# Kernel tuning notes

Measured on AMD Instinct MI355X. Metric: run time of the kernel, lower is better.

## Reference

```python
import jax, jax.numpy as jnp
import numpy as np
from jax import lax

GRID_SIZE = 5
SPLINE_ORDER = 3
N_COEF = GRID_SIZE + SPLINE_ORDER  # 8 b-spline basis functions per input
GRID_LO, GRID_HI = -1.0, 1.0


def _grid():
    h = (GRID_HI - GRID_LO) / GRID_SIZE
    return jnp.arange(-SPLINE_ORDER, GRID_SIZE + SPLINE_ORDER + 1, dtype=jnp.float32) * h + GRID_LO


def _bsplines(x):
    # x: [..., in] -> [..., in, N_COEF] via Cox-de Boor recursion (efficient-kan)
    grid = _grid()
    x = x[..., None]
    bases = ((x >= grid[:-1]) & (x < grid[1:])).astype(x.dtype)
    for j in range(1, SPLINE_ORDER + 1):
        bases = ((x - grid[:-(j + 1)]) / (grid[j:-1] - grid[:-(j + 1)]) * bases[..., :-1]
                 + (grid[j + 1:] - x) / (grid[j + 1:] - grid[1:-j]) * bases[..., 1:])
    return bases


def _kan_linear(x, base_w, spline_w):
    # x: [..., in]; base_w: [out, in]; spline_w: [out, in, N_COEF]
    base = jax.nn.silu(x) @ base_w.T
    b = _bsplines(x).reshape(x.shape[:-1] + (-1,))  # [..., in*N_COEF]
    return base + b @ spline_w.reshape(spline_w.shape[0], -1).T


def _kan_conv(x, base_w, spline_w):
    # x: [B, C, H, W]; 3x3 valid KAN convolution
    patches = lax.conv_general_dilated_patches(x, (3, 3), (1, 1), 'VALID')  # [B, C*9, H-2, W-2]
    p = patches.transpose(0, 2, 3, 1)  # [B, Ho, Wo, C*9]
    out = _kan_linear(p, base_w, spline_w)  # [B, Ho, Wo, out]
    return out.transpose(0, 3, 1, 2)


def _maxpool2(x):
    return lax.reduce_window(x, -jnp.inf, lax.max, (1, 1, 2, 2), (1, 1, 2, 2), 'VALID')


def setup_inputs() -> dict:
    key = jax.random.key(0)
    ks = jax.random.split(key, 12)
    B = 2048
    x = jax.random.uniform(ks[0], (B, 1, 28, 28), dtype=jnp.float32)
    s = 0.1
    return {
        'x': x,
        'bw1': jax.random.normal(ks[1], (5, 9), dtype=jnp.float32) * s,
        'sw1': jax.random.normal(ks[2], (5, 9, N_COEF), dtype=jnp.float32) * s,
        'bw2': jax.random.normal(ks[3], (5, 45), dtype=jnp.float32) * s,
        'sw2': jax.random.normal(ks[4], (5, 45, N_COEF), dtype=jnp.float32) * s,
        'bw3': jax.random.normal(ks[5], (2, 45), dtype=jnp.float32) * s,
        'sw3': jax.random.normal(ks[6], (2, 45, N_COEF), dtype=jnp.float32) * s,
        'w1': jax.random.normal(ks[7], (500, 162), dtype=jnp.float32) * 0.05,
        'b1': jnp.zeros((500,), dtype=jnp.float32),
        'w2': jax.random.normal(ks[8], (10, 500), dtype=jnp.float32) * 0.05,
        'b2': jnp.zeros((10,), dtype=jnp.float32),
    }


def reference(x, bw1, sw1, bw2, sw2, bw3, sw3, w1, b1, w2, b2):
    h = _kan_conv(x, bw1, sw1)       # [B, 5, 26, 26]
    h = _maxpool2(h)                 # [B, 5, 13, 13]
    h = _kan_conv(h, bw2, sw2)       # [B, 5, 11, 11]
    h = _kan_conv(h, bw3, sw3)       # [B, 2, 9, 9]
    h = h.reshape(h.shape[0], -1)    # [B, 162]
    h = jax.nn.relu(h @ w1.T + b1)   # [B, 500]
    return h @ w2.T + b2             # [B, 10]
```

## Files before the change

### kernel.cpp

```cpp
#include <hip/hip_runtime.h>


typedef _Float16 h2 __attribute__((ext_vector_type(2)));
typedef _Float16 f16x8 __attribute__((ext_vector_type(8)));
typedef float f32x4 __attribute__((ext_vector_type(4)));

union U4H { uint4 u; f16x8 h; };

__device__ __forceinline__ h2 u2h(unsigned int u) {
  union { unsigned int x; h2 h; } v; v.x = u; return v.h;
}
__device__ __forceinline__ unsigned short f2h_bits(float x) {
  union { _Float16 h; unsigned short u; } v; v.h = (_Float16)x; return v.u;
}
__device__ __forceinline__ float h2f(unsigned short u) {
  union { unsigned short u; _Float16 h; } v; v.u = u; return (float)v.h;
}
__device__ __forceinline__ unsigned int pack2h(float a, float b) {
  return (unsigned int)f2h_bits(a) | ((unsigned int)f2h_bits(b) << 16);
}
__device__ __forceinline__ float fdot2(h2 a, h2 b, float c) {
  return __builtin_amdgcn_fdot2(a, b, c, false);
}

__device__ __forceinline__ constexpr int off1(int t) {
  return (t / 3) * 28 + (t % 3);
}
__device__ __forceinline__ constexpr int off2v(int t) {
  return (t / 9) * 169 + ((t % 9) / 3) * 13 + ((t % 9) % 3);
}

__device__ __forceinline__ void featurize_regs(float v, uint4& bs, float& silu) {
  silu = v / (1.0f + __expf(-v));
  bs.x = 0u; bs.y = 0u; bs.z = 0u; bs.w = 0u;
  float u = fmaf(v, 2.5f, 5.5f);
  if (u >= 0.0f && u < 11.0f) {
    float tf = floorf(u);
    float f = u - tf, f2 = f * f, f3 = f2 * f, om = 1.0f - f;
    const float c6 = 1.0f / 6.0f;
    float w0 = om * om * om * c6;
    float w1 = (3.0f * f3 - 6.0f * f2 + 4.0f) * c6;
    float w2 = (-3.0f * f3 + 3.0f * f2 + 3.0f * f + 1.0f) * c6;
    float w3 = f3 * c6;
    unsigned long long w01 =
        (unsigned long long)f2h_bits(w0) |
        ((unsigned long long)f2h_bits(w1) << 16) |
        ((unsigned long long)f2h_bits(w2) << 32) |
        ((unsigned long long)f2h_bits(w3) << 48);
    int t = (int)tf;
    int s = 16 * t - 48;
    unsigned long long lo, hi;
    if (s >= 0) {
      lo = (s < 64) ? (w01 << s) : 0ull;
      hi = (s == 0) ? 0ull : ((s < 64) ? (w01 >> (64 - s)) : (w01 << (s - 64)));
    } else {
      lo = w01 >> (-s);
      hi = 0ull;
    }
    bs.x = (unsigned int)lo; bs.y = (unsigned int)(lo >> 32);
    bs.z = (unsigned int)hi; bs.w = (unsigned int)(hi >> 32);
  }
}

template <int NO, int CHS, int ROWW>
__device__ __forceinline__ void kconv_plain(
    const uint4* bas, const unsigned short* slu,
    const uint4* __restrict__ wS, const float* __restrict__ wB,
    int y0, int x0, float (&acc)[NO]) {
  const uint4* wp = wS;
  const float* bp = wB;
  int baC = y0 * ROWW + x0;
  #pragma unroll 1
  for (int c = 0; c < 5; ++c) {
    int ba = baC;
    #pragma unroll 1
    for (int ky = 0; ky < 3; ++ky) {
      uint4 q0 = bas[ba], q1 = bas[ba + 1], q2 = bas[ba + 2];
      float s0 = h2f(slu[ba]), s1 = h2f(slu[ba + 1]), s2 = h2f(slu[ba + 2]);
      #pragma unroll
      for (int kx = 0; kx < 3; ++kx) {
        uint4 q = (kx == 0) ? q0 : ((kx == 1) ? q1 : q2);
        float sl = (kx == 0) ? s0 : ((kx == 1) ? s1 : s2);
        h2 a0 = u2h(q.x), a1 = u2h(q.y), a2 = u2h(q.z), a3 = u2h(q.w);
        #pragma unroll
        for (int j = 0; j < NO; ++j) {
          uint4 w = wp[kx * NO + j];
          float a = acc[j];
          a = fdot2(a0, u2h(w.x), a);
          a = fdot2(a1, u2h(w.y), a);
          a = fdot2(a2, u2h(w.z), a);
          a = fdot2(a3, u2h(w.w), a);
          acc[j] = fmaf(sl, bp[kx * NO + j], a);
        }
      }
      wp += 3 * NO; bp += 3 * NO;
      ba += ROWW;
    }
    baC += CHS;
  }
}

__global__ __launch_bounds__(256) void k_prep(
    const float* __restrict__ bw1, const float* __restrict__ sw1,
    const float* __restrict__ bw2, const float* __restrict__ sw2,
    const float* __restrict__ bw3, const float* __restrict__ sw3,
    const float* __restrict__ w1, const float* __restrict__ w2,
    unsigned int* __restrict__ Bc1g, unsigned int* __restrict__ B2g,
    unsigned int* __restrict__ V3Gs, float* __restrict__ V3Gb,
    unsigned int* __restrict__ W1p4, float* __restrict__ W2p) {
  int t = blockIdx.x * 256 + threadIdx.x;
  if (t < 1280) {
    int i = t & 3, l = (t >> 2) & 63, s = t >> 8;
    int k = s * 32 + ((l >> 4) & 3) * 8 + 2 * i;
    int col = l & 15, tap = k >> 4, slot = k & 15;
    unsigned int v = 0u;
    if (col < 5 && tap < 9) {
      if (slot < 8) {
        const float* sp = sw1 + (col * 9 + tap) * 8 + slot;
        v = pack2h(sp[0], sp[1]);
      } else if (slot == 8) {
        float bv = bw1[col * 9 + tap];
        float hi = (float)(_Float16)bv;
        v = pack2h(hi, bv - hi);
      }
    }
    Bc1g[t] = v;
  }
  if (t < 5888) {
    int i = t & 3, l = (t >> 2) & 63, s = t >> 8;
    int k = s * 32 + ((l >> 4) & 3) * 8 + 2 * i;
    int col = l & 15, tap = k >> 4, slot = k & 15;
    unsigned int v = 0u;
    if (col < 5 && tap < 45) {
      if (slot < 8) {
        const float* sp = sw2 + (col * 45 + tap) * 8 + slot;
        v = pack2h(sp[0], sp[1]);
      } else if (slot == 8) {
        float bv = bw2[col * 45 + tap];
        float hi = (float)(_Float16)bv;
        v = pack2h(hi, bv - hi);
      }
    }
    B2g[t] = v;
  }
  if (t < 360) {
    int p = t & 3, u4 = t >> 2;
    int kx = u4 % 3, cky = (u4 / 3) % 15, ou = u4 / 45;
    int in = (cky / 3) * 9 + (cky % 3) * 3 + kx;
    V3Gs[t] = pack2h(sw3[(ou * 45 + in) * 8 + 2 * p], sw3[(ou * 45 + in) * 8 + 2 * p + 1]);
  }
  if (t < 90) {
    int kx = t % 3, cky = (t / 3) % 15, ou = t / 45;
    int in = (cky / 3) * 9 + (cky % 3) * 3 + kx;
    V3Gb[t] = bw3[ou * 45 + in];
  }
  if (t < 43008) {
    int j = t & 3, o = (t >> 2) & 511, g = t >> 11;
    int kp = g * 4 + j;
    W1p4[t] = (o < 500 && kp < 81)
                  ? pack2h(w1[o * 162 + 2 * kp], w1[o * 162 + 2 * kp + 1])
                  : 0u;
  }
  if (t < 5120) {
    int o = t >> 9, k = t & 511;
    W2p[t] = (k < 500) ? w2[o * 500 + k] : 0.0f;
  }
}

__global__ __launch_bounds__(256, 6) void k_fused(
    const float* __restrict__ x,
    const unsigned int* __restrict__ Bc1g, const unsigned int* __restrict__ B2g,
    const unsigned int* __restrict__ V3Gs, const float* __restrict__ V3Gb,
    const unsigned int* __restrict__ W1p4, const float* __restrict__ W2p,
    const float* __restrict__ b1, const float* __restrict__ b2,
    float* __restrict__ out) {
  __shared__ __attribute__((aligned(16))) char pool[23680];
  uint4*          RECB = (uint4*)pool;
  unsigned int*   INSP = (unsigned int*)(pool + 12544);
  uint4*          H1B  = (uint4*)pool;
  unsigned int*   H1SP = (unsigned int*)(pool + 13520);
  unsigned short* WRES = (unsigned short*)(pool + 16900);
  float*          C2   = (float*)(pool + 16900);
  uint4*          H2B  = (uint4*)pool;
  unsigned short* SLU2 = (unsigned short*)(pool + 9680);
  float*          H3F  = (float*)(pool + 16900);
  unsigned int*   HPK  = (unsigned int*)(pool + 17552);
  float*          RED  = (float*)(pool + 17888);
  unsigned int*   ZERO = (unsigned int*)(pool + 23664);
  float*          BASF = (float*)pool;

  const int b   = blockIdx.x;
  const int tid = threadIdx.x;
  const int lane = tid & 63;
  const int wv   = tid >> 6;
  const int col  = lane & 15;
  const int hi4  = lane >> 4;
  const int haf  = hi4 & 1;
  const int par  = hi4 >> 1;

  if (tid < 4) ZERO[tid] = 0u;
  #pragma unroll 1
  for (int l = tid; l < 784; l += 256) {
    uint4 bs; float sl;
    featurize_regs(x[b * 784 + l], bs, sl);
    RECB[l] = bs; INSP[l] = pack2h(sl, sl);
  }
  __syncthreads();

  {
    U4H B1[5];
    #pragma unroll
    for (int s = 0; s < 5; ++s)
      B1[s].u = ((const uint4*)Bc1g)[s * 64 + lane];
    int mt0 = wv * 11;
    int mtn = (wv < 3) ? 11 : 10;
    #pragma unroll 1
    for (int m = 0; m < mtn; ++m) {
      int mt = mt0 + m;
      int w = mt * 16 + col;
      int wc = (w < 676) ? w : 675;
      int wy = wc / 26;
      int wbase = wy * 28 + (wc - wy * 26);
      f32x4 acc = {0.f, 0.f, 0.f, 0.f};
      #pragma unroll
      for (int s = 0; s < 5; ++s) {
        const int toV = 2 * s + 1;
        int roff = par ? ((toV < 9) ? off1(toV) : 0) : off1(2 * s);
        bool valid = (!par) || (toV < 9);
        U4H a;
        if (haf == 0) {
          const uint4* ap = valid ? (RECB + (wbase + roff)) : (const uint4*)ZERO;
          a.u = *ap;
        } else {
          const unsigned int* sp = valid ? (INSP + (wbase + roff)) : ZERO;
          a.u.x = *sp; a.u.y = 0u; a.u.z = 0u; a.u.w = 0u;
        }
        acc = __builtin_amdgcn_mfma_f32_16x16x32_f16(a.h, B1[s].h, acc, 0, 0, 0);
      }
      if (col < 5) {
        #pragma unroll
        for (int r = 0; r < 4; ++r) {
          int wr = mt * 16 + hi4 * 4 + r;
          if (wr < 676) WRES[col * 676 + wr] = f2h_bits(acc[r]);
        }
      }
    }
  }
  __syncthreads();

  if (tid < 169) {
    int py = tid / 13, px = tid - (tid / 13) * 13;
    int w00 = py * 52 + px * 2;
    const unsigned int* W32 = (const unsigned int*)WRES;
    #pragma unroll
    for (int o = 0; o < 5; ++o) {
      unsigned int a = W32[(o * 676 + w00) >> 1];
      unsigned int c = W32[(o * 676 + w00 + 26) >> 1];
      float v = fmaxf(fmaxf(h2f((unsigned short)a), h2f((unsigned short)(a >> 16))),
                      fmaxf(h2f((unsigned short)c), h2f((unsigned short)(c >> 16))));
      uint4 bs; float sl;
      featurize_regs(v, bs, sl);
      H1B[o * 169 + tid] = bs;
      H1SP[o * 169 + tid] = pack2h(sl, sl);
    }
  }
  __syncthreads();

  {
    int p0 = (wv * 2) * 16 + col;
    int p1 = (wv * 2 + 1) * 16 + col;
    int pc0 = (p0 < 121) ? p0 : 120;
    int pc1 = (p1 < 121) ? p1 : 120;
    int y0 = pc0 / 11, pb0 = y0 * 13 + (pc0 - y0 * 11);
    int y1 = pc1 / 11, pb1 = y1 * 13 + (pc1 - y1 * 11);
    f32x4 ac0 = {0.f, 0.f, 0.f, 0.f}, ac1 = {0.f, 0.f, 0.f, 0.f};
    #pragma unroll
    for (int s = 0; s < 23; ++s) {
      const int toV = 2 * s + 1;
      int roff = par ? ((toV < 45) ? off2v(toV) : 0) : off2v(2 * s);
      bool valid = (!par) || (toV < 45);
      U4H bf; bf.u = ((const uint4*)B2g)[s * 64 + lane];
      U4H a0, a1;
      if (haf == 0) {
        const uint4* q0 = valid ? (H1B + (pb0 + roff)) : (const uint4*)ZERO;
        const uint4* q1 = valid ? (H1B + (pb1 + roff)) : (const uint4*)ZERO;
        a0.u = *q0; a1.u = *q1;
      } else {
        const unsigned int* s0p = valid ? (H1SP + (pb0 + roff)) : ZERO;
        const unsigned int* s1p = valid ? (H1SP + (pb1 + roff)) : ZERO;
        a0.u.x = *s0p; a0.u.y = 0u; a0.u.z = 0u; a0.u.w = 0u;
        a1.u.x = *s1p; a1.u.y = 0u; a1.u.z = 0u; a1.u.w = 0u;
      }
      ac0 = __builtin_amdgcn_mfma_f32_16x16x32_f16(a0.h, bf.h, ac0, 0, 0, 0);
      ac1 = __builtin_amdgcn_mfma_f32_16x16x32_f16(a1.h, bf.h, ac1, 0, 0, 0);
    }
    if (col < 5) {
      #pragma unroll
      for (int r = 0; r < 4; ++r) {
        C2[col * 128 + (wv * 2) * 16 + hi4 * 4 + r]     = ac0[r];
        C2[col * 128 + (wv * 2 + 1) * 16 + hi4 * 4 + r] = ac1[r];
      }
    }
  }
  __syncthreads();

  #pragma unroll 1
  for (int k2 = 0; k2 < 3; ++k2) {
    int it = tid + 256 * k2;
    if (it < 605) {
      int o = it / 121, p = it - o * 121;
      uint4 bs; float sl;
      featurize_regs(C2[o * 128 + p], bs, sl);
      H2B[o * 121 + p] = bs;
      SLU2[o * 121 + p] = f2h_bits(sl);
    }
  }
  __syncthreads();

  int og = __builtin_amdgcn_readfirstlane(tid >> 7);
  int p2 = tid & 127;
  float acc3[1] = {0.0f};
  {
    int pc = (p2 < 81) ? p2 : 80;
    int y0 = pc / 9, x0 = pc - (pc / 9) * 9;
    kconv_plain<1, 121, 11>(H2B, SLU2, (const uint4*)V3Gs + og * 45,
                            V3Gb + og * 45, y0, x0, acc3);
  }
  if (p2 < 81) H3F[og * 81 + p2] = acc3[0];
  __syncthreads();
  if (tid < 84)
    HPK[tid] = (tid < 81) ? pack2h(H3F[2 * tid], H3F[2 * tid + 1]) : 0u;
  __syncthreads();

  float fa[2] = {0.0f, 0.0f};
  {
    const uint4* hp4 = (const uint4*)HPK;
    const uint4* wbase = (const uint4*)W1p4 + tid;
    uint4 wA[2], wB[2];
    #pragma unroll
    for (int i = 0; i < 2; ++i) wA[i] = wbase[i * 256];
    #pragma unroll 1
    for (int g = 0; g < 21; g += 2) {
      if (g + 1 < 21) {
        const uint4* p = wbase + (g + 1) * 512;
        #pragma unroll
        for (int i = 0; i < 2; ++i) wB[i] = p[i * 256];
      }
      {
        uint4 hk = hp4[g];
        #pragma unroll
        for (int i = 0; i < 2; ++i) {
          float a = fa[i];
          a = fdot2(u2h(hk.x), u2h(wA[i].x), a);
          a = fdot2(u2h(hk.y), u2h(wA[i].y), a);
          a = fdot2(u2h(hk.z), u2h(wA[i].z), a);
          a = fdot2(u2h(hk.w), u2h(wA[i].w), a);
          fa[i] = a;
        }
      }
      if (g + 2 < 21) {
        const uint4* p = wbase + (g + 2) * 512;
        #pragma unroll
        for (int i = 0; i < 2; ++i) wA[i] = p[i * 256];
      }
      if (g + 1 < 21) {
        uint4 hk = hp4[g + 1];
        #pragma unroll
        for (int i = 0; i < 2; ++i) {
          float a = fa[i];
          a = fdot2(u2h(hk.x), u2h(wB[i].x), a);
          a = fdot2(u2h(hk.y), u2h(wB[i].y), a);
          a = fdot2(u2h(hk.z), u2h(wB[i].z), a);
          a = fdot2(u2h(hk.w), u2h(wB[i].w), a);
          fa[i] = a;
        }
      }
    }
  }
  #pragma unroll
  for (int i = 0; i < 2; ++i) {
    int o = tid + 256 * i;
    float bb = (o < 500) ? b1[o] : 0.0f;
    float v = fa[i] + bb;
    BASF[o] = (v > 0.0f && o < 500) ? v : 0.0f;
  }
  __syncthreads();

  float acc10[10];
  {
    float2 ha = ((const float2*)BASF)[tid];
    #pragma unroll
    for (int o = 0; o < 10; ++o) {
      float2 w = ((const float2*)&W2p[o * 512])[tid];
      acc10[o] = ha.x * w.x + ha.y * w.y;
    }
  }
  #pragma unroll
  for (int off = 32; off > 0; off >>= 1) {
    #pragma unroll
    for (int o = 0; o < 10; ++o) acc10[o] += __shfl_down(acc10[o], off);
  }
  if ((tid & 63) == 0) {
    int wid = tid >> 6;
    #pragma unroll
    for (int o = 0; o < 10; ++o) RED[wid * 10 + o] = acc10[o];
  }
  __syncthreads();
  if (tid < 10)
    out[b * 10 + tid] = RED[tid] + RED[10 + tid] + RED[20 + tid] + RED[30 + tid] + b2[tid];
}

extern "C" void kernel_launch(void* const* d_in, const int* in_sizes, int n_in,
                              void* d_out, int out_size, void* d_ws, size_t ws_size,
                              hipStream_t stream) {
  (void)in_sizes; (void)n_in; (void)out_size; (void)ws_size;
  const float* x   = (const float*)d_in[0];
  const float* bw1 = (const float*)d_in[1];
  const float* sw1 = (const float*)d_in[2];
  const float* bw2 = (const float*)d_in[3];
  const float* sw2 = (const float*)d_in[4];
  const float* bw3 = (const float*)d_in[5];
  const float* sw3 = (const float*)d_in[6];
  const float* w1  = (const float*)d_in[7];
  const float* b1  = (const float*)d_in[8];
  const float* w2  = (const float*)d_in[9];
  const float* b2  = (const float*)d_in[10];
  float* out = (float*)d_out;

  char* ws = (char*)d_ws;
  unsigned int* Bc1g = (unsigned int*)(ws);
  unsigned int* B2g  = (unsigned int*)(ws + 5120);
  unsigned int* V3Gs = (unsigned int*)(ws + 28672);
  float*        V3Gb = (float*)(ws + 30112);
  float*        W2p  = (float*)(ws + 30720);
  unsigned int* W1p4 = (unsigned int*)(ws + 51200);

  k_prep<<<168, 256, 0, stream>>>(bw1, sw1, bw2, sw2, bw3, sw3, w1, w2,
                                  Bc1g, B2g, V3Gs, V3Gb, W1p4, W2p);
  k_fused<<<2048, 256, 0, stream>>>(x, Bc1g, B2g, V3Gs, V3Gb,
                                    W1p4, W2p, b1, b2, out);
}
```

Before: 130.5 us.

## Move third KAN conv to MFMA and drop zero-pointer select in tap loops

Replaces the scalar fdot2-based third KAN convolution with a 16x16x32 f16 MFMA implicit-GEMM over 81 positions, using a packed B3 weight matrix prepared in k_prep that holds spline and split-precision base weights. Stores silu values duplicated as packed half pairs so the hi/lo base weight trick works in the MFMA k-slot. Also simplifies the tap offset computation for conv1/conv2 by mapping padded taps to offset 0 instead of selecting a zero buffer, relying on zero weights to null them. This moves layer-3 work onto the matrix cores but pads 2 outputs to 16 columns, wasting most of each MFMA, and leaves waves unevenly loaded across two passes.

Measured after the change: 137.4 us. +5.3%, slower.

```diff
diff --git a/kernel.cpp b/kernel.cpp
--- a/kernel.cpp
+++ b/kernel.cpp
@@ -23,11 +23,14 @@
   return __builtin_amdgcn_fdot2(a, b, c, false);
 }
 
-__device__ __forceinline__ constexpr int off1(int t) {
-  return (t / 3) * 28 + (t % 3);
-}
-__device__ __forceinline__ constexpr int off2v(int t) {
-  return (t / 9) * 169 + ((t % 9) / 3) * 13 + ((t % 9) % 3);
+__device__ __forceinline__ constexpr int off1t(int t) {
+  return (t >= 9) ? 0 : (t / 3) * 28 + (t % 3);
+}
+__device__ __forceinline__ constexpr int off2t(int t) {
+  return (t >= 45) ? 0 : (t / 9) * 169 + ((t % 9) / 3) * 13 + (t % 9) % 3;
+}
+__device__ __forceinline__ constexpr int off3t(int t) {
+  return (t >= 45) ? 0 : (t / 9) * 121 + ((t % 9) / 3) * 11 + (t % 9) % 3;
 }
 
 __device__ __forceinline__ void featurize_regs(float v, uint4& bs, float& silu) {
@@ -62,51 +65,13 @@
   }
 }
 
-template <int NO, int CHS, int ROWW>
-__device__ __forceinline__ void kconv_plain(
-    const uint4* bas, const unsigned short* slu,
-    const uint4* __restrict__ wS, const float* __restrict__ wB,
-    int y0, int x0, float (&acc)[NO]) {
-  const uint4* wp = wS;
-  const float* bp = wB;
-  int baC = y0 * ROWW + x0;
-  #pragma unroll 1
-  for (int c = 0; c < 5; ++c) {
-    int ba = baC;
-    #pragma unroll 1
-    for (int ky = 0; ky < 3; ++ky) {
-      uint4 q0 = bas[ba], q1 = bas[ba + 1], q2 = bas[ba + 2];
-      float s0 = h2f(slu[ba]), s1 = h2f(slu[ba + 1]), s2 = h2f(slu[ba + 2]);
-      #pragma unroll
-      for (int kx = 0; kx < 3; ++kx) {
-        uint4 q = (kx == 0) ? q0 : ((kx == 1) ? q1 : q2);
-        float sl = (kx == 0) ? s0 : ((kx == 1) ? s1 : s2);
-        h2 a0 = u2h(q.x), a1 = u2h(q.y), a2 = u2h(q.z), a3 = u2h(q.w);
-        #pragma unroll
-        for (int j = 0; j < NO; ++j) {
-          uint4 w = wp[kx * NO + j];
-          float a = acc[j];
-          a = fdot2(a0, u2h(w.x), a);
-          a = fdot2(a1, u2h(w.y), a);
-          a = fdot2(a2, u2h(w.z), a);
-          a = fdot2(a3, u2h(w.w), a);
-          acc[j] = fmaf(sl, bp[kx * NO + j], a);
-        }
-      }
-      wp += 3 * NO; bp += 3 * NO;
-      ba += ROWW;
-    }
-    baC += CHS;
-  }
-}
-
 __global__ __launch_bounds__(256) void k_prep(
     const float* __restrict__ bw1, const float* __restrict__ sw1,
     const float* __restrict__ bw2, const float* __restrict__ sw2,
     const float* __restrict__ bw3, const float* __restrict__ sw3,
     const float* __restrict__ w1, const float* __restrict__ w2,
     unsigned int* __restrict__ Bc1g, unsigned int* __restrict__ B2g,
-    unsigned int* __restrict__ V3Gs, float* __restrict__ V3Gb,
+    unsigned int* __restrict__ B3g,
     unsigned int* __restrict__ W1p4, float* __restrict__ W2p) {
   int t = blockIdx.x * 256 + threadIdx.x;
   if (t < 1280) {
@@ -143,16 +108,22 @@
     }
     B2g[t] = v;
   }
-  if (t < 360) {
-    int p = t & 3, u4 = t >> 2;
-    int kx = u4 % 3, cky = (u4 / 3) % 15, ou = u4 / 45;
-    int in = (cky / 3) * 9 + (cky % 3) * 3 + kx;
-    V3Gs[t] = pack2h(sw3[(ou * 45 + in) * 8 + 2 * p], sw3[(ou * 45 + in) * 8 + 2 * p + 1]);
-  }
-  if (t < 90) {
-    int kx = t % 3, cky = (t / 3) % 15, ou = t / 45;
-    int in = (cky / 3) * 9 + (cky % 3) * 3 + kx;
-    V3Gb[t] = bw3[ou * 45 + in];
+  if (t < 5888) {
+    int i = t & 3, l = (t >> 2) & 63, s = t >> 8;
+    int k = s * 32 + ((l >> 4) & 3) * 8 + 2 * i;
+    int col = l & 15, tap = k >> 4, slot = k & 15;
+    unsigned int v = 0u;
+    if (col < 2 && tap < 45) {
+      if (slot < 8) {
+        const float* sp = sw3 + (col * 45 + tap) * 8 + slot;
+        v = pack2h(sp[0], sp[1]);
+      } else if (slot == 8) {
+        float bv = bw3[col * 45 + tap];
+        float hi = (float)(_Float16)bv;
+        v = pack2h(hi, bv - hi);
+      }
+    }
+    B3g[t] = v;
   }
   if (t < 43008) {
     int j = t & 3, o = (t >> 2) & 511, g = t >> 11;
@@ -170,7 +141,7 @@
 __global__ __launch_bounds__(256, 6) void k_fused(
     const float* __restrict__ x,
     const unsigned int* __restrict__ Bc1g, const unsigned int* __restrict__ B2g,
-    const unsigned int* __restrict__ V3Gs, const float* __restrict__ V3Gb,
+    const unsigned int* __restrict__ B3g,
     const unsigned int* __restrict__ W1p4, const float* __restrict__ W2p,
     const float* __restrict__ b1, const float* __restrict__ b2,
     float* __restrict__ out) {
@@ -182,11 +153,10 @@
   unsigned short* WRES = (unsigned short*)(pool + 16900);
   float*          C2   = (float*)(pool + 16900);
   uint4*          H2B  = (uint4*)pool;
-  unsigned short* SLU2 = (unsigned short*)(pool + 9680);
+  unsigned int*   SP2  = (unsigned int*)(pool + 9680);
   float*          H3F  = (float*)(pool + 16900);
   unsigned int*   HPK  = (unsigned int*)(pool + 17552);
   float*          RED  = (float*)(pool + 17888);
-  unsigned int*   ZERO = (unsigned int*)(pool + 23664);
   float*          BASF = (float*)pool;
 
   const int b   = blockIdx.x;
@@ -198,7 +168,6 @@
   const int haf  = hi4 & 1;
   const int par  = hi4 >> 1;
 
-  if (tid < 4) ZERO[tid] = 0u;
   #pragma unroll 1
   for (int l = tid; l < 784; l += 256) {
     uint4 bs; float sl;
@@ -224,16 +193,12 @@
       f32x4 acc = {0.f, 0.f, 0.f, 0.f};
       #pragma unroll
       for (int s = 0; s < 5; ++s) {
-        const int toV = 2 * s + 1;
-        int roff = par ? ((toV < 9) ? off1(toV) : 0) : off1(2 * s);
-        bool valid = (!par) || (toV < 9);
+        int ro = par ? off1t(2 * s + 1) : off1t(2 * s);
         U4H a;
         if (haf == 0) {
-          const uint4* ap = valid ? (RECB + (wbase + roff)) : (const uint4*)ZERO;
-          a.u = *ap;
+          a.u = RECB[wbase + ro];
         } else {
-          const unsigned int* sp = valid ? (INSP + (wbase + roff)) : ZERO;
-          a.u.x = *sp; a.u.y = 0u; a.u.z = 0u; a.u.w = 0u;
+          a.u.x = INSP[wbase + ro]; a.u.y = 0u; a.u.z = 0u; a.u.w = 0u;
         }
         acc = __builtin_amdgcn_mfma_f32_16x16x32_f16(a.h, B1[s].h, acc, 0, 0, 0);
       }
@@ -276,20 +241,14 @@
     f32x4 ac0 = {0.f, 0.f, 0.f, 0.f}, ac1 = {0.f, 0.f, 0.f, 0.f};
     #pragma unroll
     for (int s = 0; s < 23; ++s) {
-      const int toV = 2 * s + 1;
-      int roff = par ? ((toV < 45) ? off2v(toV) : 0) : off2v(2 * s);
-      bool valid = (!par) || (toV < 45);
+      int ro = par ? off2t(2 * s + 1) : off2t(2 * s);
       U4H bf; bf.u = ((const uint4*)B2g)[s * 64 + lane];
       U4H a0, a1;
       if (haf == 0) {
-        const uint4* q0 = valid ? (H1B + (pb0 + roff)) : (const uint4*)ZERO;
-        const uint4* q1 = valid ? (H1B + (pb1 + roff)) : (const uint4*)ZERO;
-        a0.u = *q0; a1.u = *q1;
+        a0.u = H1B[pb0 + ro]; a1.u = H1B[pb1 + ro];
       } else {
-        const unsigned int* s0p = valid ? (H1SP + (pb0 + roff)) : ZERO;
-        const unsigned int* s1p = valid ? (H1SP + (pb1 + roff)) : ZERO;
-        a0.u.x = *s0p; a0.u.y = 0u; a0.u.z = 0u; a0.u.w = 0u;
-        a1.u.x = *s1p; a1.u.y = 0u; a1.u.z = 0u; a1.u.w = 0u;
+        a0.u.x = H1SP[pb0 + ro]; a0.u.y = 0u; a0.u.z = 0u; a0.u.w = 0u;
+        a1.u.x = H1SP[pb1 + ro]; a1.u.y = 0u; a1.u.z = 0u; a1.u.w = 0u;
       }
       ac0 = __builtin_amdgcn_mfma_f32_16x16x32_f16(a0.h, bf.h, ac0, 0, 0, 0);
       ac1 = __builtin_amdgcn_mfma_f32_16x16x32_f16(a1.h, bf.h, ac1, 0, 0, 0);
@@ -312,21 +271,42 @@
       uint4 bs; float sl;
       featurize_regs(C2[o * 128 + p], bs, sl);
       H2B[o * 121 + p] = bs;
-      SLU2[o * 121 + p] = f2h_bits(sl);
-    }
-  }
-  __syncthreads();
-
-  int og = __builtin_amdgcn_readfirstlane(tid >> 7);
-  int p2 = tid & 127;
-  float acc3[1] = {0.0f};
+      SP2[o * 121 + p] = pack2h(sl, sl);
+    }
+  }
+  __syncthreads();
+
   {
-    int pc = (p2 < 81) ? p2 : 80;
-    int y0 = pc / 9, x0 = pc - (pc / 9) * 9;
-    kconv_plain<1, 121, 11>(H2B, SLU2, (const uint4*)V3Gs + og * 45,
-                            V3Gb + og * 45, y0, x0, acc3);
-  }
-  if (p2 < 81) H3F[og * 81 + p2] = acc3[0];
+    #pragma unroll 1
+    for (int pass = 0; pass < 2; ++pass) {
+      if (pass == 1 && wv >= 2) break;
+      int mt = (pass == 0) ? wv : (wv + 4);
+      int pos = mt * 16 + col;
+      int pc = (pos < 81) ? pos : 80;
+      int y0 = pc / 9;
+      int pb = y0 * 11 + (pc - y0 * 9);
+      f32x4 acc = {0.f, 0.f, 0.f, 0.f};
+      #pragma unroll
+      for (int s = 0; s < 23; ++s) {
+        int ro = par ? off3t(2 * s + 1) : off3t(2 * s);
+        U4H bf; bf.u = ((const uint4*)B3g)[s * 64 + lane];
+        U4H a;
+        if (haf == 0) {
+          a.u = H2B[pb + ro];
+        } else {
+          a.u.x = SP2[pb + ro]; a.u.y = 0u; a.u.z = 0u; a.u.w = 0u;
+        }
+        acc = __builtin_amdgcn_mfma_f32_16x16x32_f16(a.h, bf.h, acc, 0, 0, 0);
+      }
+      if (col < 2) {
+        #pragma unroll
+        for (int r = 0; r < 4; ++r) {
+          int pr = mt * 16 + hi4 * 4 + r;
+          if (pr < 81) H3F[col * 81 + pr] = acc[r];
+        }
+      }
+    }
+  }
   __syncthreads();
   if (tid < 84)
     HPK[tid] = (tid < 81) ? pack2h(H3F[2 * tid], H3F[2 * tid + 1]) : 0u;
@@ -430,13 +410,12 @@
   char* ws = (char*)d_ws;
   unsigned int* Bc1g = (unsigned int*)(ws);
   unsigned int* B2g  = (unsigned int*)(ws + 5120);
-  unsigned int* V3Gs = (unsigned int*)(ws + 28672);
-  float*        V3Gb = (float*)(ws + 30112);
-  float*        W2p  = (float*)(ws + 30720);
-  unsigned int* W1p4 = (unsigned int*)(ws + 51200);
+  unsigned int* B3g  = (unsigned int*)(ws + 28672);
+  float*        W2p  = (float*)(ws + 52224);
+  unsigned int* W1p4 = (unsigned int*)(ws + 73728);
 
   k_prep<<<168, 256, 0, stream>>>(bw1, sw1, bw2, sw2, bw3, sw3, w1, w2,
-                                  Bc1g, B2g, V3Gs, V3Gb, W1p4, W2p);
-  k_fused<<<2048, 256, 0, stream>>>(x, Bc1g, B2g, V3Gs, V3Gb,
+                                  Bc1g, B2g, B3g, W1p4, W2p);
+  k_fused<<<2048, 256, 0, stream>>>(x, Bc1g, B2g, B3g,
                                     W1p4, W2p, b1, b2, out);
 }
```
